# Kernel optimization log

Hardware: AMD Instinct MI355X
Metric: run time of the kernel (lower is better)

Reference implementation:

```python
import jax, jax.numpy as jnp
import numpy as np

D_MODEL, N_HEAD, N_KV_HEAD, D_HEAD = 1024, 16, 4, 64


def rotate_half(x):
    x1, x2 = x[..., : x.shape[-1] // 2], x[..., x.shape[-1] // 2:]
    return jnp.concatenate((-x2, x1), axis=-1)


def rope_cos_sin(seq_len, dim, dtype=jnp.float32):
    inv_freq = 1.0 / (10000.0 ** (jnp.arange(0, dim, 2, dtype=jnp.float32) / dim))
    t = jnp.arange(seq_len, dtype=jnp.float32)
    freqs = jnp.einsum('i,j->ij', t, inv_freq)          # [S, dim/2]
    emb = jnp.concatenate((freqs, freqs), axis=-1)       # [S, dim]
    return jnp.cos(emb).astype(dtype), jnp.sin(emb).astype(dtype)


def setup_inputs() -> dict:
    key = jax.random.key(0)
    ks = jax.random.split(key, 5)
    B, S = 2, 2048
    scale = 0.02
    return {
        'x': jax.random.normal(ks[0], (B, S, D_MODEL), dtype=jnp.float32),
        'Wq': jax.random.normal(ks[1], (D_MODEL, N_HEAD * D_HEAD), dtype=jnp.float32) * scale,
        'Wk': jax.random.normal(ks[2], (D_MODEL, N_KV_HEAD * D_HEAD), dtype=jnp.float32) * scale,
        'Wv': jax.random.normal(ks[3], (D_MODEL, N_KV_HEAD * D_HEAD), dtype=jnp.float32) * scale,
        'Wo': jax.random.normal(ks[4], (N_HEAD * D_HEAD, D_MODEL), dtype=jnp.float32) * scale,
    }


def reference(x, Wq, Wk, Wv, Wo):
    B, S, _ = x.shape
    scale = 1.0 / np.sqrt(D_HEAD)
    # projections -> [B, H, S, Dh]
    q = (x @ Wq).reshape(B, S, N_HEAD, D_HEAD).transpose(0, 2, 1, 3)
    k = (x @ Wk).reshape(B, S, N_KV_HEAD, D_HEAD).transpose(0, 2, 1, 3)
    v = (x @ Wv).reshape(B, S, N_KV_HEAD, D_HEAD).transpose(0, 2, 1, 3)
    cos, sin = rope_cos_sin(S, D_HEAD, x.dtype)          # [S, Dh]
    q = q * cos + rotate_half(q) * sin
    k = k * cos + rotate_half(k) * sin
    rep = N_HEAD // N_KV_HEAD
    k = jnp.repeat(k, rep, axis=1)                       # [B, H, S, Dh]
    v = jnp.repeat(v, rep, axis=1)
    scores = jnp.einsum('bhqd,bhkd->bhqk', q, k) * scale # [B, H, S, S]
    causal = jnp.triu(jnp.ones((S, S), dtype=bool), k=1)
    scores = jnp.where(causal, -jnp.inf, scores)
    probs = jax.nn.softmax(scores, axis=-1)
    ctx = jnp.einsum('bhqk,bhkd->bhqd', probs, v)        # [B, H, S, Dh]
    ctx = ctx.transpose(0, 2, 1, 3).reshape(B, S, N_HEAD * D_HEAD)
    return ctx @ Wo
```

## Files before the change

### kernel.cpp

```cpp
#include <hip/hip_runtime.h>
#include <hip/hip_bf16.h>
#include <cstdint>
#include <math.h>

#define S_LEN 2048
#define DM 1024
#define NQKV 1536
#define MROWS 4096

typedef __attribute__((ext_vector_type(8))) short short8;
typedef __attribute__((ext_vector_type(4))) float f32x4;
typedef __attribute__((ext_vector_type(16))) float f32x16;

#define QFOLD 0.18033688011112042f

__device__ __forceinline__ short f2bf(float x) {
  union { float f; uint32_t u; } v; v.f = x;
  uint32_t r = (v.u + 0x7fffu + ((v.u >> 16) & 1u)) >> 16;
  return (short)(uint16_t)r;
}

__device__ __forceinline__ uint32_t pk2(float a, float b) {
  __hip_bfloat162 h = __float22bfloat162_rn(make_float2(a, b));
  union { __hip_bfloat162 h2; uint32_t u; } cv; cv.h2 = h;
  return cv.u;
}

__global__ void f32_to_bf16_vec(const float* __restrict__ in, short* __restrict__ out, int n4) {
  int i = blockIdx.x * blockDim.x + threadIdx.x;
  if (i < n4) {
    float4 v = ((const float4*)in)[i];
    short4 o;
    o.x = f2bf(v.x); o.y = f2bf(v.y); o.z = f2bf(v.z); o.w = f2bf(v.w);
    ((short4*)out)[i] = o;
  }
}

__global__ __launch_bounds__(256) void transpose_f32_bf16(const float* __restrict__ src,
    short* __restrict__ dst, int R, int C) {
  __shared__ short T[64 * 72];
  const int r0 = blockIdx.x * 64, c0 = blockIdx.y * 64;
  const int tid = threadIdx.x;
  #pragma unroll
  for (int i = 0; i < 4; ++i) {
    int chunk = tid + i * 256;
    int r = chunk >> 4, cc = (chunk & 15) * 4;
    float4 v = *(const float4*)&src[(size_t)(r0 + r) * C + c0 + cc];
    T[(cc + 0) * 72 + r] = f2bf(v.x);
    T[(cc + 1) * 72 + r] = f2bf(v.y);
    T[(cc + 2) * 72 + r] = f2bf(v.z);
    T[(cc + 3) * 72 + r] = f2bf(v.w);
  }
  __syncthreads();
  #pragma unroll
  for (int i = 0; i < 2; ++i) {
    int chunk = tid + i * 256;
    int rr = chunk >> 3, kk = (chunk & 7) * 8;
    *(uint4*)&dst[(size_t)(c0 + rr) * R + r0 + kk] = *(uint4*)&T[rr * 72 + kk];
  }
}

#define BM 128
#define BN 128
#define BKT 64

__global__ __launch_bounds__(256) void gemm_bf16(const short* __restrict__ A,
    const short* __restrict__ BT, float* __restrict__ C, int M, int N, int K) {
  __shared__ short As[BM * BKT];
  __shared__ short Bs[BN * BKT];
  const int tid = threadIdx.x;
  const int wave = tid >> 6, lane = tid & 63;
  const int quad = lane >> 4, l15 = lane & 15;
  const int wm = (wave >> 1) * 64, wn = (wave & 1) * 64;
  const int m0 = blockIdx.y * BM, n0 = blockIdx.x * BN;

  const int sr = wave * 32 + (lane >> 3);
  const int scol = (lane & 7) * 8;

  f32x4 acc[4][4] = {};

  for (int k0 = 0; k0 < K; k0 += BKT) {
    __syncthreads();
    #pragma unroll
    for (int j = 0; j < 4; ++j) {
      const int r = sr + j * 8;
      __builtin_amdgcn_global_load_lds(
          (const __attribute__((address_space(1))) void*)&A[(size_t)(m0 + r) * K + k0 + scol],
          (__attribute__((address_space(3))) void*)&As[(wave * 4 + j) * 512],
          16, 0, 0);
      __builtin_amdgcn_global_load_lds(
          (const __attribute__((address_space(1))) void*)&BT[(size_t)(n0 + r) * K + k0 + scol],
          (__attribute__((address_space(3))) void*)&Bs[(wave * 4 + j) * 512],
          16, 0, 0);
    }
    __syncthreads();
    #pragma unroll
    for (int ks = 0; ks < 2; ++ks) {
      short8 af[4], bfr[4];
      #pragma unroll
      for (int mi = 0; mi < 4; ++mi)
        af[mi] = *(const short8*)&As[(wm + mi*16 + l15)*BKT + ks*32 + quad*8];
      #pragma unroll
      for (int ni = 0; ni < 4; ++ni)
        bfr[ni] = *(const short8*)&Bs[(wn + ni*16 + l15)*BKT + ks*32 + quad*8];
      #pragma unroll
      for (int mi = 0; mi < 4; ++mi)
        #pragma unroll
        for (int ni = 0; ni < 4; ++ni)
          acc[mi][ni] = __builtin_amdgcn_mfma_f32_16x16x32_bf16(af[mi], bfr[ni], acc[mi][ni], 0, 0, 0);
    }
  }
  #pragma unroll
  for (int mi = 0; mi < 4; ++mi)
    #pragma unroll
    for (int ni = 0; ni < 4; ++ni)
      #pragma unroll
      for (int r = 0; r < 4; ++r)
        C[(size_t)(m0 + wm + mi*16 + quad*4 + r)*N + (n0 + wn + ni*16 + l15)] = acc[mi][ni][r];
}

__global__ void rope_kernel(const float* __restrict__ qkv, short* __restrict__ Qb,
                            short* __restrict__ Kb, short* __restrict__ Vb) {
  __shared__ float csn[64];
  const int row = blockIdx.x;
  const int s = row & (S_LEN - 1);
  const int tid = threadIdx.x;
  const float* rp = qkv + (size_t)row * NQKV;
  if (tid < 32) {
    float inv = exp2f(-(float)tid * 0.41524101186092029f);
    float ang = (float)s * inv;
    csn[tid] = cosf(ang);
    csn[tid + 32] = sinf(ang);
  }
  __syncthreads();
  #pragma unroll
  for (int i = 0; i < 2; ++i) {
    int p = tid + i * 256;
    int hh = p >> 5, j = p & 31;
    float cs = csn[j], sn = csn[j + 32];
    float x1 = rp[hh*64 + j], x2 = rp[hh*64 + j + 32];
    Qb[(size_t)row*1024 + hh*64 + j]      = f2bf((x1*cs - x2*sn) * QFOLD);
    Qb[(size_t)row*1024 + hh*64 + j + 32] = f2bf((x2*cs + x1*sn) * QFOLD);
  }
  if (tid < 128) {
    int hh = tid >> 5, j = tid & 31;
    float cs = csn[j], sn = csn[j + 32];
    float x1 = rp[1024 + hh*64 + j], x2 = rp[1024 + hh*64 + j + 32];
    const int sw = (s & 7) << 3;
    Kb[(size_t)row*256 + hh*64 + (j ^ sw)]        = f2bf(x1*cs - x2*sn);
    Kb[(size_t)row*256 + hh*64 + ((j + 32) ^ sw)] = f2bf(x2*cs + x1*sn);
  }
  Vb[(size_t)row*256 + tid] = f2bf(rp[1280 + tid]);
}

__global__ __launch_bounds__(256) void transpose_v(const short* __restrict__ Vb,
                                                   short* __restrict__ Vt) {
  __shared__ short T[64 * 72];
  const int s0 = blockIdx.x * 64;
  const int bh = blockIdx.y;
  const int b = bh >> 2, kvh = bh & 3;
  const int tid = threadIdx.x;
  #pragma unroll
  for (int i = 0; i < 2; ++i) {
    int chunk = tid + i * 256;
    int r = chunk >> 3, c = (chunk & 7) * 8;
    short8 v = *(const short8*)&Vb[(size_t)(b*S_LEN + s0 + r)*256 + kvh*64 + c];
    #pragma unroll
    for (int t = 0; t < 8; ++t) T[(c + t) * 72 + r] = v[t];
  }
  __syncthreads();
  #pragma unroll
  for (int i = 0; i < 2; ++i) {
    int chunk = tid + i * 256;
    int rr = chunk >> 3, kk = (chunk & 7) * 8;
    *(uint4*)&Vt[(size_t)(bh*64 + rr)*S_LEN + s0 + (kk ^ ((rr & 7) << 3))] = *(uint4*)&T[rr * 72 + kk];
  }
}

__global__ __launch_bounds__(256, 2) void fattn8(const short* __restrict__ Qb,
    const short* __restrict__ Kb, const short* __restrict__ Vt, short* __restrict__ Ctx) {
  __shared__ short SMEM[32768];
  const int idx = blockIdx.x;
  const int pi  = idx & 15;
  const int h   = (idx >> 4) & 15;
  const int b   = idx >> 8;
  const int kvh = h >> 2;
  const int tid = threadIdx.x, wav = tid >> 6, lane = tid & 63;
  const int l31 = lane & 31, hi = lane >> 5;
  const int qs = wav & 1, g = wav >> 1;
  const int sx = (l31 & 7) << 3;
  const size_t qbase  = (size_t)b * S_LEN * 1024;
  const size_t kbase  = (size_t)b * S_LEN * 256;
  const size_t vtbase = (size_t)(b * 4 + kvh) * 64 * S_LEN;

  const short* kptr = Kb + kbase + (size_t)(wav * 32 + (lane >> 3)) * 256 + kvh * 64 + (lane & 7) * 8;
  const short* vptr = Vt + vtbase + (size_t)(wav * 16 + (lane >> 4)) * 2048 + (lane & 15) * 8;

#define STAGE(bi, k0s) do { \
    const short* kp_ = kptr + (size_t)(k0s) * 256; \
    const short* vp_ = vptr + (k0s); \
    short* kd_ = &SMEM[(bi) * 8192 + wav * 2048]; \
    short* vd_ = &SMEM[16384 + (bi) * 8192 + wav * 2048]; \
    _Pragma("unroll") \
    for (int i_ = 0; i_ < 4; ++i_) { \
      __builtin_amdgcn_global_load_lds((const __attribute__((address_space(1))) void*)(kp_ + i_ * 2048), \
          (__attribute__((address_space(3))) void*)(kd_ + i_ * 512), 16, 0, 0); \
      __builtin_amdgcn_global_load_lds((const __attribute__((address_space(1))) void*)(vp_ + i_ * 8192), \
          (__attribute__((address_space(3))) void*)(vd_ + i_ * 512), 16, 0, 0); \
    } \
  } while (0)

  for (int half = 0; half < 2; ++half) {
    const int jt = half ? (31 - pi) : pi;
    const int q0 = jt * 64;
    const int ntiles = (jt >> 1) + 1;
    const int qg = q0 + qs * 32 + l31;

    short8 qf[4];
    {
      const short* qp = &Qb[qbase + (size_t)qg * 1024 + h * 64 + hi * 8];
      #pragma unroll
      for (int ks = 0; ks < 4; ++ks) qf[ks] = *(const short8*)(qp + ks * 16);
    }

    f32x16 O0 = {}, O1 = {};
    float la0 = 0.f, la1 = 0.f, la2 = 0.f, la3 = 0.f;

    STAGE(0, 0);
    __syncthreads();

    for (int t = 0; t < ntiles; ++t) {
      const int cur = t & 1;
      const int k0 = t * 128;
      if (t + 1 < ntiles) STAGE((t + 1) & 1, (t + 1) * 128);

      const short* ks_ = &SMEM[cur * 8192];
      const short* vs_ = &SMEM[16384 + cur * 8192];

      f32x16 sc[2];
      __builtin_amdgcn_s_setprio(1);
      #pragma unroll
      for (int kt = 0; kt < 2; ++kt) {
        const int r = g * 64 + kt * 32 + l31;
        f32x16 a = {};
        #pragma unroll
        for (int ks2 = 0; ks2 < 4; ++ks2) {
          short8 kf = *(const short8*)&ks_[r * 64 + ((ks2 * 16 + hi * 8) ^ sx)];
          a = __builtin_amdgcn_mfma_f32_32x32x16_bf16(kf, qf[ks2], a, 0, 0, 0);
        }
        sc[kt] = a;
      }
      __builtin_amdgcn_s_setprio(0);

      if (t == ntiles - 1) {
        #pragma unroll
        for (int kt = 0; kt < 2; ++kt)
          #pragma unroll
          for (int r = 0; r < 16; ++r) {
            const int kvg = k0 + g * 64 + kt * 32 + (r & 3) + 8 * (r >> 2) + 4 * hi;
            if (kvg > qg) sc[kt][r] = -1e30f;
          }
      }

      short8 af[4];
      #pragma unroll
      for (int kt = 0; kt < 2; ++kt) {
        #pragma unroll
        for (int r = 0; r < 16; ++r) sc[kt][r] = exp2f(sc[kt][r]);
        la0 += (sc[kt][0] + sc[kt][1]) + (sc[kt][2] + sc[kt][3]);
        la1 += (sc[kt][4] + sc[kt][5]) + (sc[kt][6] + sc[kt][7]);
        la2 += (sc[kt][8] + sc[kt][9]) + (sc[kt][10] + sc[kt][11]);
        la3 += (sc[kt][12] + sc[kt][13]) + (sc[kt][14] + sc[kt][15]);
        #pragma unroll
        for (int st = 0; st < 2; ++st) {
          uint32_t x0 = pk2(sc[kt][st * 8 + 0], sc[kt][st * 8 + 1]);
          uint32_t x1 = pk2(sc[kt][st * 8 + 2], sc[kt][st * 8 + 3]);
          uint32_t x2 = pk2(sc[kt][st * 8 + 4], sc[kt][st * 8 + 5]);
          uint32_t x3 = pk2(sc[kt][st * 8 + 6], sc[kt][st * 8 + 7]);
          asm("v_permlane32_swap_b32 %0, %1" : "+v"(x0), "+v"(x2));
          asm("v_permlane32_swap_b32 %0, %1" : "+v"(x1), "+v"(x3));
          union { short8 s8; uint32_t u[4]; } cv;
          cv.u[0] = x0; cv.u[1] = x1; cv.u[2] = x2; cv.u[3] = x3;
          af[kt * 2 + st] = cv.s8;
        }
      }

      __builtin_amdgcn_s_setprio(1);
      #pragma unroll
      for (int s = 0; s < 4; ++s) {
        const int co = g * 64 + s * 16 + hi * 8;
        short8 bv0 = *(const short8*)&vs_[l31 * 128 + (co ^ sx)];
        O0 = __builtin_amdgcn_mfma_f32_32x32x16_bf16(af[s], bv0, O0, 0, 0, 0);
        short8 bv1 = *(const short8*)&vs_[(32 + l31) * 128 + (co ^ sx)];
        O1 = __builtin_amdgcn_mfma_f32_32x32x16_bf16(af[s], bv1, O1, 0, 0, 0);
      }
      __builtin_amdgcn_s_setprio(0);

      __syncthreads();
    }

    float ll = (la0 + la1) + (la2 + la3);
    ll += __shfl_xor(ll, 32, 64);

    float* Os = (float*)SMEM;
    float* Ls = (float*)SMEM + 2 * 64 * 33;
    if (g == 0) {
      float* op = &Os[(qs * 64 + lane) * 33];
      #pragma unroll
      for (int r = 0; r < 16; ++r) { op[r] = O0[r]; op[16 + r] = O1[r]; }
      Ls[qs * 64 + lane] = ll;
    }
    __syncthreads();
    if (g == 1) {
      const float lt = ll + Ls[qs * 64 + lane];
      const float inv = 1.0f / lt;
      const float* op = &Os[(qs * 64 + lane) * 33];
      #pragma unroll
      for (int r = 0; r < 16; ++r) { O0[r] += op[r]; O1[r] += op[16 + r]; }
      #pragma unroll
      for (int r = 0; r < 16; ++r) {
        const int crow = (r & 3) + 8 * (r >> 2) + 4 * hi;
        const float invr = __shfl(inv, crow, 64);
        const size_t o = qbase + (size_t)(q0 + qs * 32 + crow) * 1024 + h * 64;
        Ctx[o + l31]      = f2bf(O0[r] * invr);
        Ctx[o + 32 + l31] = f2bf(O1[r] * invr);
      }
    }
    __syncthreads();
  }
#undef STAGE
}

extern "C" void kernel_launch(void* const* d_in, const int* in_sizes, int n_in,
                              void* d_out, int out_size, void* d_ws, size_t ws_size,
                              hipStream_t stream) {
  const float* x  = (const float*)d_in[0];
  const float* Wq = (const float*)d_in[1];
  const float* Wk = (const float*)d_in[2];
  const float* Wv = (const float*)d_in[3];
  const float* Wo = (const float*)d_in[4];
  float* out = (float*)d_out;

  char* w = (char*)d_ws;
  short* Xb    = (short*)w;  w += (size_t)MROWS * DM * 2;
  short* WcatT = (short*)w;  w += (size_t)NQKV * DM * 2;
  short* WoT   = (short*)w;  w += (size_t)DM * DM * 2;
  float* QKVf  = (float*)w;  w += (size_t)MROWS * NQKV * 4;
  short* Qbuf  = (short*)w;  w += (size_t)MROWS * DM * 2;
  short* Kbuf  = (short*)w;  w += (size_t)MROWS * 256 * 2;
  short* Vbuf  = (short*)w;  w += (size_t)MROWS * 256 * 2;
  short* Vt    = (short*)w;  w += (size_t)8 * 64 * S_LEN * 2;
  short* Ctx   = (short*)QKVf;

  f32_to_bf16_vec<<<dim3(4096), dim3(256), 0, stream>>>(x, Xb, MROWS * DM / 4);
  transpose_f32_bf16<<<dim3(16, 16), dim3(256), 0, stream>>>(Wq, WcatT, 1024, 1024);
  transpose_f32_bf16<<<dim3(16, 4),  dim3(256), 0, stream>>>(Wk, WcatT + (size_t)1024*1024, 1024, 256);
  transpose_f32_bf16<<<dim3(16, 4),  dim3(256), 0, stream>>>(Wv, WcatT + (size_t)1280*1024, 1024, 256);
  transpose_f32_bf16<<<dim3(16, 16), dim3(256), 0, stream>>>(Wo, WoT, 1024, 1024);

  gemm_bf16<<<dim3(NQKV / BN, MROWS / BM), dim3(256), 0, stream>>>(Xb, WcatT, QKVf, MROWS, NQKV, DM);
  rope_kernel<<<dim3(MROWS), dim3(256), 0, stream>>>(QKVf, Qbuf, Kbuf, Vbuf);
  transpose_v<<<dim3(32, 8), dim3(256), 0, stream>>>(Vbuf, Vt);
  fattn8<<<dim3(512), dim3(256), 0, stream>>>(Qbuf, Kbuf, Vt, Ctx);
  gemm_bf16<<<dim3(DM / BN, MROWS / BM), dim3(256), 0, stream>>>(Ctx, WoT, out, MROWS, DM, DM);
}
```

Before: 191.8 us.

## Split attention KV tile across four wave groups and shrink GEMM tiles

The flash-attention kernel now runs 512 threads per block instead of 256. Each of four wave groups handles 32 of the 128 keys in a tile rather than 64, and the partial O and row sums are combined through shared memory in a three-way reduction at the end. Both GEMMs switch to a templated kernel with 64x128 tiles, which launches more blocks to fill the CUs better. The cost is a larger end-of-block reduction, fewer MFMAs per wave per tile, and more register pressure under the (512,4) launch bound.

```diff
diff --git a/kernel.cpp b/kernel.cpp
--- a/kernel.cpp
+++ b/kernel.cpp
@@ -7,6 +7,7 @@
 #define DM 1024
 #define NQKV 1536
 #define MROWS 4096
+#define BKT 64
 
 typedef __attribute__((ext_vector_type(8))) short short8;
 typedef __attribute__((ext_vector_type(4))) float f32x4;
@@ -60,60 +61,58 @@
   }
 }
 
-#define BM 128
-#define BN 128
-#define BKT 64
-
-__global__ __launch_bounds__(256) void gemm_bf16(const short* __restrict__ A,
+template<int BMT, int BNT>
+__global__ __launch_bounds__(256) void gemm_bf16_t(const short* __restrict__ A,
     const short* __restrict__ BT, float* __restrict__ C, int M, int N, int K) {
-  __shared__ short As[BM * BKT];
-  __shared__ short Bs[BN * BKT];
+  constexpr int MI = BMT / 32, NI = BNT / 32;
+  __shared__ short As[BMT * BKT];
+  __shared__ short Bs[BNT * BKT];
   const int tid = threadIdx.x;
   const int wave = tid >> 6, lane = tid & 63;
   const int quad = lane >> 4, l15 = lane & 15;
-  const int wm = (wave >> 1) * 64, wn = (wave & 1) * 64;
-  const int m0 = blockIdx.y * BM, n0 = blockIdx.x * BN;
-
-  const int sr = wave * 32 + (lane >> 3);
+  const int wm = (wave >> 1) * (BMT / 2), wn = (wave & 1) * (BNT / 2);
+  const int m0 = blockIdx.y * BMT, n0 = blockIdx.x * BNT;
+  const int rA = wave * (BMT / 4) + (lane >> 3);
+  const int rB = wave * (BNT / 4) + (lane >> 3);
   const int scol = (lane & 7) * 8;
 
-  f32x4 acc[4][4] = {};
+  f32x4 acc[MI][NI] = {};
 
   for (int k0 = 0; k0 < K; k0 += BKT) {
     __syncthreads();
     #pragma unroll
-    for (int j = 0; j < 4; ++j) {
-      const int r = sr + j * 8;
+    for (int j = 0; j < MI; ++j)
       __builtin_amdgcn_global_load_lds(
-          (const __attribute__((address_space(1))) void*)&A[(size_t)(m0 + r) * K + k0 + scol],
-          (__attribute__((address_space(3))) void*)&As[(wave * 4 + j) * 512],
+          (const __attribute__((address_space(1))) void*)&A[(size_t)(m0 + rA + j * 8) * K + k0 + scol],
+          (__attribute__((address_space(3))) void*)&As[(wave * MI + j) * 512],
           16, 0, 0);
+    #pragma unroll
+    for (int j = 0; j < NI; ++j)
       __builtin_amdgcn_global_load_lds(
-          (const __attribute__((address_space(1))) void*)&BT[(size_t)(n0 + r) * K + k0 + scol],
-          (__attribute__((address_space(3))) void*)&Bs[(wave * 4 + j) * 512],
+          (const __attribute__((address_space(1))) void*)&BT[(size_t)(n0 + rB + j * 8) * K + k0 + scol],
+          (__attribute__((address_space(3))) void*)&Bs[(wave * NI + j) * 512],
           16, 0, 0);
-    }
     __syncthreads();
     #pragma unroll
     for (int ks = 0; ks < 2; ++ks) {
-      short8 af[4], bfr[4];
-      #pragma unroll
-      for (int mi = 0; mi < 4; ++mi)
+      short8 af[MI], bfr[NI];
+      #pragma unroll
+      for (int mi = 0; mi < MI; ++mi)
         af[mi] = *(const short8*)&As[(wm + mi*16 + l15)*BKT + ks*32 + quad*8];
       #pragma unroll
-      for (int ni = 0; ni < 4; ++ni)
+      for (int ni = 0; ni < NI; ++ni)
         bfr[ni] = *(const short8*)&Bs[(wn + ni*16 + l15)*BKT + ks*32 + quad*8];
       #pragma unroll
-      for (int mi = 0; mi < 4; ++mi)
-        #pragma unroll
-        for (int ni = 0; ni < 4; ++ni)
+      for (int mi = 0; mi < MI; ++mi)
+        #pragma unroll
+        for (int ni = 0; ni < NI; ++ni)
           acc[mi][ni] = __builtin_amdgcn_mfma_f32_16x16x32_bf16(af[mi], bfr[ni], acc[mi][ni], 0, 0, 0);
     }
   }
   #pragma unroll
-  for (int mi = 0; mi < 4; ++mi)
-    #pragma unroll
-    for (int ni = 0; ni < 4; ++ni)
+  for (int mi = 0; mi < MI; ++mi)
+    #pragma unroll
+    for (int ni = 0; ni < NI; ++ni)
       #pragma unroll
       for (int r = 0; r < 4; ++r)
         C[(size_t)(m0 + wm + mi*16 + quad*4 + r)*N + (n0 + wn + ni*16 + l15)] = acc[mi][ni][r];
@@ -177,7 +176,7 @@
   }
 }
 
-__global__ __launch_bounds__(256, 2) void fattn8(const short* __restrict__ Qb,
+__global__ __launch_bounds__(512, 4) void fattn9(const short* __restrict__ Qb,
     const short* __restrict__ Kb, const short* __restrict__ Vt, short* __restrict__ Ctx) {
   __shared__ short SMEM[32768];
   const int idx = blockIdx.x;
@@ -193,16 +192,16 @@
   const size_t kbase  = (size_t)b * S_LEN * 256;
   const size_t vtbase = (size_t)(b * 4 + kvh) * 64 * S_LEN;
 
-  const short* kptr = Kb + kbase + (size_t)(wav * 32 + (lane >> 3)) * 256 + kvh * 64 + (lane & 7) * 8;
-  const short* vptr = Vt + vtbase + (size_t)(wav * 16 + (lane >> 4)) * 2048 + (lane & 15) * 8;
+  const short* kptr = Kb + kbase + (size_t)(wav * 16 + (lane >> 3)) * 256 + kvh * 64 + (lane & 7) * 8;
+  const short* vptr = Vt + vtbase + (size_t)(wav * 8 + (lane >> 4)) * 2048 + (lane & 15) * 8;
 
 #define STAGE(bi, k0s) do { \
     const short* kp_ = kptr + (size_t)(k0s) * 256; \
     const short* vp_ = vptr + (k0s); \
-    short* kd_ = &SMEM[(bi) * 8192 + wav * 2048]; \
-    short* vd_ = &SMEM[16384 + (bi) * 8192 + wav * 2048]; \
+    short* kd_ = &SMEM[(bi) * 8192 + wav * 1024]; \
+    short* vd_ = &SMEM[16384 + (bi) * 8192 + wav * 1024]; \
     _Pragma("unroll") \
-    for (int i_ = 0; i_ < 4; ++i_) { \
+    for (int i_ = 0; i_ < 2; ++i_) { \
       __builtin_amdgcn_global_load_lds((const __attribute__((address_space(1))) void*)(kp_ + i_ * 2048), \
           (__attribute__((address_space(3))) void*)(kd_ + i_ * 512), 16, 0, 0); \
       __builtin_amdgcn_global_load_lds((const __attribute__((address_space(1))) void*)(vp_ + i_ * 8192), \
@@ -237,58 +236,54 @@
       const short* ks_ = &SMEM[cur * 8192];
       const short* vs_ = &SMEM[16384 + cur * 8192];
 
-      f32x16 sc[2];
+      f32x16 sc;
       __builtin_amdgcn_s_setprio(1);
-      #pragma unroll
-      for (int kt = 0; kt < 2; ++kt) {
-        const int r = g * 64 + kt * 32 + l31;
+      {
+        const int r = g * 32 + l31;
         f32x16 a = {};
         #pragma unroll
         for (int ks2 = 0; ks2 < 4; ++ks2) {
           short8 kf = *(const short8*)&ks_[r * 64 + ((ks2 * 16 + hi * 8) ^ sx)];
           a = __builtin_amdgcn_mfma_f32_32x32x16_bf16(kf, qf[ks2], a, 0, 0, 0);
         }
-        sc[kt] = a;
+        sc = a;
       }
       __builtin_amdgcn_s_setprio(0);
 
       if (t == ntiles - 1) {
         #pragma unroll
-        for (int kt = 0; kt < 2; ++kt)
-          #pragma unroll
-          for (int r = 0; r < 16; ++r) {
-            const int kvg = k0 + g * 64 + kt * 32 + (r & 3) + 8 * (r >> 2) + 4 * hi;
-            if (kvg > qg) sc[kt][r] = -1e30f;
-          }
-      }
-
-      short8 af[4];
-      #pragma unroll
-      for (int kt = 0; kt < 2; ++kt) {
-        #pragma unroll
-        for (int r = 0; r < 16; ++r) sc[kt][r] = exp2f(sc[kt][r]);
-        la0 += (sc[kt][0] + sc[kt][1]) + (sc[kt][2] + sc[kt][3]);
-        la1 += (sc[kt][4] + sc[kt][5]) + (sc[kt][6] + sc[kt][7]);
-        la2 += (sc[kt][8] + sc[kt][9]) + (sc[kt][10] + sc[kt][11]);
-        la3 += (sc[kt][12] + sc[kt][13]) + (sc[kt][14] + sc[kt][15]);
+        for (int r = 0; r < 16; ++r) {
+          const int kvg = k0 + g * 32 + (r & 3) + 8 * (r >> 2) + 4 * hi;
+          if (kvg > qg) sc[r] = -1e30f;
+        }
+      }
+
+      short8 af[2];
+      {
+        #pragma unroll
+        for (int r = 0; r < 16; ++r) sc[r] = exp2f(sc[r]);
+        la0 += (sc[0] + sc[1]) + (sc[2] + sc[3]);
+        la1 += (sc[4] + sc[5]) + (sc[6] + sc[7]);
+        la2 += (sc[8] + sc[9]) + (sc[10] + sc[11]);
+        la3 += (sc[12] + sc[13]) + (sc[14] + sc[15]);
         #pragma unroll
         for (int st = 0; st < 2; ++st) {
-          uint32_t x0 = pk2(sc[kt][st * 8 + 0], sc[kt][st * 8 + 1]);
-          uint32_t x1 = pk2(sc[kt][st * 8 + 2], sc[kt][st * 8 + 3]);
-          uint32_t x2 = pk2(sc[kt][st * 8 + 4], sc[kt][st * 8 + 5]);
-          uint32_t x3 = pk2(sc[kt][st * 8 + 6], sc[kt][st * 8 + 7]);
+          uint32_t x0 = pk2(sc[st * 8 + 0], sc[st * 8 + 1]);
+          uint32_t x1 = pk2(sc[st * 8 + 2], sc[st * 8 + 3]);
+          uint32_t x2 = pk2(sc[st * 8 + 4], sc[st * 8 + 5]);
+          uint32_t x3 = pk2(sc[st * 8 + 6], sc[st * 8 + 7]);
           asm("v_permlane32_swap_b32 %0, %1" : "+v"(x0), "+v"(x2));
           asm("v_permlane32_swap_b32 %0, %1" : "+v"(x1), "+v"(x3));
           union { short8 s8; uint32_t u[4]; } cv;
           cv.u[0] = x0; cv.u[1] = x1; cv.u[2] = x2; cv.u[3] = x3;
-          af[kt * 2 + st] = cv.s8;
+          af[st] = cv.s8;
         }
       }
 
       __builtin_amdgcn_s_setprio(1);
       #pragma unroll
-      for (int s = 0; s < 4; ++s) {
-        const int co = g * 64 + s * 16 + hi * 8;
+      for (int s = 0; s < 2; ++s) {
+        const int co = g * 32 + s * 16 + hi * 8;
         short8 bv0 = *(const short8*)&vs_[l31 * 128 + (co ^ sx)];
         O0 = __builtin_amdgcn_mfma_f32_32x32x16_bf16(af[s], bv0, O0, 0, 0, 0);
         short8 bv1 = *(const short8*)&vs_[(32 + l31) * 128 + (co ^ sx)];
@@ -303,20 +298,23 @@
     ll += __shfl_xor(ll, 32, 64);
 
     float* Os = (float*)SMEM;
-    float* Ls = (float*)SMEM + 2 * 64 * 33;
+    float* Ls = (float*)SMEM + 2 * 3 * 64 * 33;
+    if (g > 0) {
+      float* op = &Os[((qs * 3 + (g - 1)) * 64 + lane) * 33];
+      #pragma unroll
+      for (int r = 0; r < 16; ++r) { op[r] = O0[r]; op[16 + r] = O1[r]; }
+      Ls[(qs * 3 + (g - 1)) * 64 + lane] = ll;
+    }
+    __syncthreads();
     if (g == 0) {
-      float* op = &Os[(qs * 64 + lane) * 33];
-      #pragma unroll
-      for (int r = 0; r < 16; ++r) { op[r] = O0[r]; op[16 + r] = O1[r]; }
-      Ls[qs * 64 + lane] = ll;
-    }
-    __syncthreads();
-    if (g == 1) {
-      const float lt = ll + Ls[qs * 64 + lane];
-      const float inv = 1.0f / lt;
-      const float* op = &Os[(qs * 64 + lane) * 33];
-      #pragma unroll
-      for (int r = 0; r < 16; ++r) { O0[r] += op[r]; O1[r] += op[16 + r]; }
+      #pragma unroll
+      for (int src = 0; src < 3; ++src) {
+        const float* op = &Os[((qs * 3 + src) * 64 + lane) * 33];
+        #pragma unroll
+        for (int r = 0; r < 16; ++r) { O0[r] += op[r]; O1[r] += op[16 + r]; }
+        ll += Ls[(qs * 3 + src) * 64 + lane];
+      }
+      const float inv = 1.0f / ll;
       #pragma unroll
       for (int r = 0; r < 16; ++r) {
         const int crow = (r & 3) + 8 * (r >> 2) + 4 * hi;
@@ -358,9 +356,9 @@
   transpose_f32_bf16<<<dim3(16, 4),  dim3(256), 0, stream>>>(Wv, WcatT + (size_t)1280*1024, 1024, 256);
   transpose_f32_bf16<<<dim3(16, 16), dim3(256), 0, stream>>>(Wo, WoT, 1024, 1024);
 
-  gemm_bf16<<<dim3(NQKV / BN, MROWS / BM), dim3(256), 0, stream>>>(Xb, WcatT, QKVf, MROWS, NQKV, DM);
+  gemm_bf16_t<64,128><<<dim3(NQKV / 128, MROWS / 64), dim3(256), 0, stream>>>(Xb, WcatT, QKVf, MROWS, NQKV, DM);
   rope_kernel<<<dim3(MROWS), dim3(256), 0, stream>>>(QKVf, Qbuf, Kbuf, Vbuf);
   transpose_v<<<dim3(32, 8), dim3(256), 0, stream>>>(Vbuf, Vt);
-  fattn8<<<dim3(512), dim3(256), 0, stream>>>(Qbuf, Kbuf, Vt, Ctx);
-  gemm_bf16<<<dim3(DM / BN, MROWS / BM), dim3(256), 0, stream>>>(Ctx, WoT, out, MROWS, DM, DM);
-}
+  fattn9<<<dim3(512), dim3(512), 0, stream>>>(Qbuf, Kbuf, Vt, Ctx);
+  gemm_bf16_t<64,128><<<dim3(DM / 128, MROWS / 64), dim3(256), 0, stream>>>(Ctx, WoT, out, MROWS, DM, DM);
+}
```

After: 185.3 us. -3.4%, faster.
